# Performance work log

Measured on AMD Instinct MI355X. Metric: run time of the kernel, lower is better.

## Reference

```python
import jax, jax.numpy as jnp
import numpy as np

N = 50000      # num_nodes
E = 800000     # num_edges
D = 128        # node feature dim
ED = 64        # edge feature dim
H = 4          # num_heads
U = 32         # units per head (units*heads == 128)


def setup_inputs() -> dict:
    key = jax.random.key(0)
    ks = jax.random.split(key, 12)
    inputs = jax.random.normal(ks[0], (N, D), dtype=jnp.float32)
    # tf.math.segment_* requires sorted segment ids -> sort source row
    src = jnp.sort(jax.random.randint(ks[1], (E,), 0, N, dtype=jnp.int32))
    dst = jax.random.randint(ks[2], (E,), 0, N, dtype=jnp.int32)
    edge_index = jnp.stack([src, dst], axis=0)
    edge_features = jax.random.normal(ks[3], (E, ED), dtype=jnp.float32)
    def glorot(k, shape):
        lim = np.sqrt(6.0 / (shape[0] + shape[1]))
        return jax.random.uniform(k, shape, jnp.float32, -lim, lim)
    HU = H * U
    return {
        "inputs": inputs,
        "edge_index": edge_index,
        "edge_features": edge_features,
        "Wq": glorot(ks[4], (D, HU)), "bq": jnp.zeros((HU,), jnp.float32),
        "Wk": glorot(ks[5], (D, HU)), "bk": jnp.zeros((HU,), jnp.float32),
        "Wv": glorot(ks[6], (D, HU)), "bv": jnp.zeros((HU,), jnp.float32),
        "We": glorot(ks[7], (ED, HU)), "be": jnp.zeros((HU,), jnp.float32),
        "Wo": glorot(ks[8], (HU, U)), "bo": jnp.zeros((U,), jnp.float32),
    }


def _segment_softmax(scores, seg, num_segments):
    # numerically stable segmented softmax over ragged neighborhoods
    seg_max = jax.ops.segment_max(scores, seg, num_segments=num_segments)
    ex = jnp.exp(scores - seg_max[seg])
    seg_sum = jax.ops.segment_sum(ex, seg, num_segments=num_segments)
    return ex / seg_sum[seg]


def reference(inputs, edge_index, edge_features, Wq, bq, Wk, bk, Wv, bv, We, be, Wo, bo):
    n = inputs.shape[0]
    q = (inputs @ Wq + bq).reshape(n, H, U)
    k = (inputs @ Wk + bk).reshape(n, H, U)
    v = (inputs @ Wv + bv).reshape(n, H, U)
    src, dst = edge_index[0], edge_index[1]
    qi = q[src]                      # [E, H, U]
    kj = k[dst]                      # [E, H, U]
    scores = jnp.sum(qi * kj, axis=-1)   # [E, H]
    eh = (edge_features @ We + be).reshape(-1, H, U)
    scores = scores + jnp.sum(eh * kj, axis=-1)
    attn = _segment_softmax(scores, src, n)        # [E, H]
    attended = jax.ops.segment_sum(attn[..., None] * v[dst], src, num_segments=n)
    attended = attended.reshape(n, H * U)
    return jax.nn.relu(attended @ Wo + bo)
```

## Files before the change

kernel.cpp:

```cpp
#include <hip/hip_runtime.h>
#include <math.h>

#define N_NODES 50000
#define N_EDGES 800000
#define D_IN    128
#define ED_IN   64
#define HU      128
#define NH      4
#define UD      32

typedef float fx4 __attribute__((ext_vector_type(4)));
typedef short s16x8 __attribute__((ext_vector_type(8)));
typedef float f32x4 __attribute__((ext_vector_type(4)));

static __device__ __forceinline__ unsigned short f2bf(float f) {
  unsigned u = __float_as_uint(f);
  unsigned r = (u + 0x7FFFu + ((u >> 16) & 1u)) >> 16;
  return (unsigned short)r;
}
static __device__ __forceinline__ float bf_lo(unsigned u) {
  return __uint_as_float(u << 16);
}
static __device__ __forceinline__ float bf_hi(unsigned u) {
  return __uint_as_float(u & 0xFFFF0000u);
}
static __device__ __forceinline__ float bf2f(unsigned short h) {
  return __uint_as_float(((unsigned)h) << 16);
}
static __device__ __forceinline__ float dot8(float4 a0, float4 a1, uint4 kk) {
  return a0.x * bf_lo(kk.x) + a0.y * bf_hi(kk.x)
       + a0.z * bf_lo(kk.y) + a0.w * bf_hi(kk.y)
       + a1.x * bf_lo(kk.z) + a1.y * bf_hi(kk.z)
       + a1.z * bf_lo(kk.w) + a1.w * bf_hi(kk.w);
}
static __device__ __forceinline__ float4 f4add(float4 a, float4 b) {
  return make_float4(a.x + b.x, a.y + b.y, a.z + b.z, a.w + b.w);
}

__global__ __launch_bounds__(256) void offsets_kernel(
    const int* __restrict__ src, int* __restrict__ off) {
  const int e = blockIdx.x * 256 + threadIdx.x;
  if (e >= N_EDGES) return;
  const int s = src[e];
  const int prev = (e == 0) ? -1 : src[e - 1];
  for (int n = prev + 1; n <= s; ++n) off[n] = e;
  if (e == N_EDGES - 1)
    for (int n = s + 1; n <= N_NODES; ++n) off[n] = N_EDGES;
}

__global__ __launch_bounds__(256) void wepack_kernel(
    const float* __restrict__ We, unsigned short* __restrict__ wf) {
  const int fl = blockIdx.x * 256 + threadIdx.x;
  if (fl >= 16 * 64) return;
  const int f = fl >> 6, lane = fl & 63;
  const int nt = f >> 1, kh = f & 1;
  const int n = nt * 16 + (lane & 15);
  const int kbase = kh * 32 + (lane >> 4) * 8;
#pragma unroll
  for (int j = 0; j < 8; ++j)
    wf[fl * 8 + j] = f2bf(We[(kbase + j) * HU + n]);
}

__global__ __launch_bounds__(256) void wqkvpack_kernel(
    const float* __restrict__ Wq, const float* __restrict__ Wk,
    const float* __restrict__ Wv, unsigned short* __restrict__ wqkv) {
  const int fl = blockIdx.x * 256 + threadIdx.x;
  if (fl >= 96 * 64) return;
  const int f = fl >> 6, lane = fl & 63;
  const int proj = f >> 5, nt = (f >> 2) & 7, kf = f & 3;
  const float* W = proj == 0 ? Wq : (proj == 1 ? Wk : Wv);
  const int n = nt * 16 + (lane & 15);
  const int kb = kf * 32 + (lane >> 4) * 8;
#pragma unroll
  for (int j = 0; j < 8; ++j) {
    const float v = W[(kb + j) * HU + n];
    const unsigned short h = f2bf(v);
    wqkv[fl * 8 + j] = h;
    wqkv[96 * 64 * 8 + fl * 8 + j] = f2bf(v - bf2f(h));
  }
}

__global__ __launch_bounds__(256) void qkv_kernel(
    const float* __restrict__ x, const s16x8* __restrict__ wqkv,
    const float* __restrict__ bq, const float* __restrict__ be,
    const float* __restrict__ bk, const float* __restrict__ bv,
    float* __restrict__ q, unsigned short* __restrict__ kbf,
    unsigned short* __restrict__ vbf) {
  const int base = blockIdx.x * 16;
  const int t = threadIdx.x;
  const int w = t >> 6, l = t & 63;

  const float* xr = x + (long)(base + (l & 15)) * D_IN + (l >> 4) * 8;
  s16x8 Ah[4], Al[4];
#pragma unroll
  for (int kf = 0; kf < 4; ++kf) {
    const fx4 c0 = *(const fx4*)(xr + kf * 32);
    const fx4 c1 = *(const fx4*)(xr + kf * 32 + 4);
#pragma unroll
    for (int j = 0; j < 4; ++j) {
      const unsigned short h0 = f2bf(c0[j]);
      const unsigned short h1 = f2bf(c1[j]);
      Ah[kf][j] = (short)h0;     Al[kf][j] = (short)f2bf(c0[j] - bf2f(h0));
      Ah[kf][4 + j] = (short)h1; Al[kf][4 + j] = (short)f2bf(c1[j] - bf2f(h1));
    }
  }

#pragma unroll
  for (int i = 0; i < 6; ++i) {
    const int tt = w * 6 + i;
    const int proj = tt >> 3, nt = tt & 7;
    const int col = nt * 16 + (l & 15);
    f32x4 acc = (f32x4){0.f, 0.f, 0.f, 0.f};
#pragma unroll
    for (int kf = 0; kf < 4; ++kf) {
      const int fr = proj * 32 + nt * 4 + kf;
      const s16x8 Bh = wqkv[fr * 64 + l];
      const s16x8 Bl = wqkv[96 * 64 + fr * 64 + l];
      acc = __builtin_amdgcn_mfma_f32_16x16x32_bf16(Ah[kf], Bh, acc, 0, 0, 0);
      acc = __builtin_amdgcn_mfma_f32_16x16x32_bf16(Al[kf], Bh, acc, 0, 0, 0);
      acc = __builtin_amdgcn_mfma_f32_16x16x32_bf16(Ah[kf], Bl, acc, 0, 0, 0);
    }
    float bias;
    if (proj == 0)      bias = bq[col] + be[col];
    else if (proj == 1) bias = bk[col];
    else                bias = bv[col];
#pragma unroll
    for (int r = 0; r < 4; ++r) {
      const long node = base + (l >> 4) * 4 + r;
      const float val = acc[r] + bias;
      if (proj == 0)      q[node * HU + col] = val;
      else if (proj == 1) kbf[node * HU + col] = f2bf(val);
      else                vbf[node * HU + col] = f2bf(val);
    }
  }
}

__global__ __launch_bounds__(256) void score_kernel(
    const float* __restrict__ ef,
    const int* __restrict__ src, const int* __restrict__ dst,
    const float* __restrict__ q, const unsigned short* __restrict__ kbf,
    const s16x8* __restrict__ wf,
    float* __restrict__ scores) {
  __shared__ __align__(16) float ehs[4][16 * 64];
  const int t = threadIdx.x;
  const int w = t >> 6, l = t & 63;
  const long ebase = (long)blockIdx.x * 64;
  const int e = (int)(ebase + w * 16 + (l >> 2));
  const int hl = (l >> 1) & 1, half = l & 1;
  const int s = src[e], d = dst[e];

  const char* kbp = (const char*)kbf + (long)d * 256 + hl * 64 + half * 32;
  const uint4 k00 = *(const uint4*)(kbp);
  const uint4 k01 = *(const uint4*)(kbp + 16);
  const uint4 k10 = *(const uint4*)(kbp + 128);
  const uint4 k11 = *(const uint4*)(kbp + 144);

  const int arow = (int)(ebase + w * 16 + (l & 15));
  const fx4* ap = (const fx4*)(ef + (long)arow * ED_IN + (l >> 4) * 8);
  const fx4 a00 = __builtin_nontemporal_load(ap);
  const fx4 a01 = __builtin_nontemporal_load(ap + 1);
  const fx4 a10 = __builtin_nontemporal_load(ap + 8);
  const fx4 a11 = __builtin_nontemporal_load(ap + 9);
  s16x8 A0, A1;
  A0[0] = (short)f2bf(a00[0]); A0[1] = (short)f2bf(a00[1]);
  A0[2] = (short)f2bf(a00[2]); A0[3] = (short)f2bf(a00[3]);
  A0[4] = (short)f2bf(a01[0]); A0[5] = (short)f2bf(a01[1]);
  A0[6] = (short)f2bf(a01[2]); A0[7] = (short)f2bf(a01[3]);
  A1[0] = (short)f2bf(a10[0]); A1[1] = (short)f2bf(a10[1]);
  A1[2] = (short)f2bf(a10[2]); A1[3] = (short)f2bf(a10[3]);
  A1[4] = (short)f2bf(a11[0]); A1[5] = (short)f2bf(a11[1]);
  A1[6] = (short)f2bf(a11[2]); A1[7] = (short)f2bf(a11[3]);

  float* __restrict__ ehw = ehs[w];
  const int nb = l & 15, gbase = (l >> 4) * 4;
  const int rloc = l >> 2;
  const int swzr = (rloc & 7) << 4;

#pragma unroll
  for (int ph = 0; ph < 2; ++ph) {
    f32x4 acc[4];
#pragma unroll
    for (int ntl = 0; ntl < 4; ++ntl) acc[ntl] = (f32x4){0.f, 0.f, 0.f, 0.f};
#pragma unroll
    for (int ntl = 0; ntl < 4; ++ntl) {
      const int f = (ph * 4 + ntl) * 2;
      const s16x8 B0 = wf[(f + 0) * 64 + l];
      const s16x8 B1 = wf[(f + 1) * 64 + l];
      acc[ntl] = __builtin_amdgcn_mfma_f32_16x16x32_bf16(A0, B0, acc[ntl], 0, 0, 0);
      acc[ntl] = __builtin_amdgcn_mfma_f32_16x16x32_bf16(A1, B1, acc[ntl], 0, 0, 0);
    }

#pragma unroll
    for (int ntl = 0; ntl < 4; ++ntl) {
#pragma unroll
      for (int r = 0; r < 4; ++r) {
        const int m = gbase + r;
        const int b = (ntl * 16 + nb) * 4;
        ehw[(m * 256 + (b ^ ((m & 7) << 4))) >> 2] = acc[ntl][r];
      }
    }
    asm volatile("s_waitcnt lgkmcnt(0)" ::: "memory");
    __builtin_amdgcn_sched_barrier(0x30);

    const int h = ph * 2 + hl;
    const char* ehp = (const char*)(ehw + rloc * 64);
    const int cb = (l & 3) * 64;
    const float4 e0 = *(const float4*)(ehp + ((cb + 0)  ^ swzr));
    const float4 e1 = *(const float4*)(ehp + ((cb + 16) ^ swzr));
    const float4 e2 = *(const float4*)(ehp + ((cb + 32) ^ swzr));
    const float4 e3 = *(const float4*)(ehp + ((cb + 48) ^ swzr));

    const float4* qp = (const float4*)(q + (long)s * HU + h * 32 + half * 16);
    const float4 q0 = qp[0], q1 = qp[1], q2 = qp[2], q3 = qp[3];
    const uint4 k0 = ph ? k10 : k00;
    const uint4 k1 = ph ? k11 : k01;

    float p = dot8(f4add(q0, e0), f4add(q1, e1), k0)
            + dot8(f4add(q2, e2), f4add(q3, e3), k1);
    p += __shfl_xor(p, 1, 64);
    if (!half)
      __builtin_nontemporal_store(p, scores + (long)e * NH + h);

    asm volatile("s_waitcnt lgkmcnt(0)" ::: "memory");
    __builtin_amdgcn_sched_barrier(0x30);
  }
}

__global__ __launch_bounds__(256) void aggregate_kernel(
    const int* __restrict__ off, const int* __restrict__ dst,
    const float* __restrict__ scores, const unsigned* __restrict__ v2,
    const float* __restrict__ Wo, const float* __restrict__ bo,
    float* __restrict__ out) {
  const int wv = threadIdx.x >> 6, l = threadIdx.x & 63;
  const int n = blockIdx.x * 4 + wv;
  const int h = l >> 4, q16 = l & 15;
  __shared__ float att[4][HU];
  __shared__ __align__(16) float wos[HU * UD];

  {
    const fx4* wop = (const fx4*)Wo;
    fx4* wosp = (fx4*)wos;
#pragma unroll
    for (int r = 0; r < 4; ++r)
      wosp[threadIdx.x + 256 * r] = wop[threadIdx.x + 256 * r];
  }
  __syncthreads();

  const int start = off[n], end = off[n + 1];
  float m = -INFINITY, lsum = 0.f, a0 = 0.f, a1 = 0.f;
  for (int cs = start; cs < end; cs += 16) {
    const int e = cs + q16;
    const bool live = (e < end);
    const float sc = live ? __builtin_nontemporal_load(scores + (long)e * NH + h)
                          : -INFINITY;
    const int dl = live ? dst[e] : 0;
    float mc = sc;
#pragma unroll
    for (int o = 8; o > 0; o >>= 1) mc = fmaxf(mc, __shfl_xor(mc, o, 16));
    const float nm = fmaxf(m, mc);
    const float corr = __expf(m - nm);
    const float w = __expf(sc - nm);
    float ws = w;
#pragma unroll
    for (int o = 8; o > 0; o >>= 1) ws += __shfl_xor(ws, o, 16);
    lsum = lsum * corr + ws;
    a0 *= corr; a1 *= corr; m = nm;
#pragma unroll
    for (int j = 0; j < 16; ++j) {
      const float wj = __shfl(w, (l & 48) + j, 64);
      const int dj = __builtin_amdgcn_readlane(dl, j);
      const unsigned vr = v2[(long)dj * 64 + l];
      a0 += wj * bf_lo(vr);
      a1 += wj * bf_hi(vr);
    }
  }
  const float inv = (lsum > 0.f) ? 1.f / lsum : 0.f;
  att[wv][2 * l] = a0 * inv;
  att[wv][2 * l + 1] = a1 * inv;
  const int o = l & 31, half = l >> 5;
  float po = 0.f;
#pragma unroll
  for (int f = 0; f < 64; ++f)
    po += att[wv][half * 64 + f] * wos[(half * 64 + f) * UD + o];
  po += __shfl_down(po, 32, 64);
  if (l < 32) out[(long)n * UD + l] = fmaxf(po + bo[l], 0.f);
}

extern "C" void kernel_launch(void* const* d_in, const int* in_sizes, int n_in,
                              void* d_out, int out_size, void* d_ws, size_t ws_size,
                              hipStream_t stream) {
  const float* x  = (const float*)d_in[0];
  const int*   ei = (const int*)d_in[1];
  const float* ef = (const float*)d_in[2];
  const float* Wq = (const float*)d_in[3];
  const float* bq = (const float*)d_in[4];
  const float* Wk = (const float*)d_in[5];
  const float* bk = (const float*)d_in[6];
  const float* Wv = (const float*)d_in[7];
  const float* bv = (const float*)d_in[8];
  const float* We = (const float*)d_in[9];
  const float* be = (const float*)d_in[10];
  const float* Wo = (const float*)d_in[11];
  const float* bo = (const float*)d_in[12];
  float* out = (float*)d_out;

  const int* src = ei;
  const int* dst = ei + N_EDGES;

  float* q = (float*)d_ws;
  unsigned short* kbf = (unsigned short*)(q + (long)N_NODES * HU);
  unsigned short* vbf = kbf + (long)N_NODES * HU;
  float* scores = (float*)(vbf + (long)N_NODES * HU);
  int* off = (int*)(scores + (long)N_EDGES * NH);
  unsigned short* wf = (unsigned short*)(((uintptr_t)(off + N_NODES + 1) + 15)
                                         & ~(uintptr_t)15);
  unsigned short* wqkv = wf + 16 * 64 * 8;

  offsets_kernel<<<(N_EDGES + 255) / 256, 256, 0, stream>>>(src, off);
  wepack_kernel<<<4, 256, 0, stream>>>(We, wf);
  wqkvpack_kernel<<<24, 256, 0, stream>>>(Wq, Wk, Wv, wqkv);
  qkv_kernel<<<N_NODES / 16, 256, 0, stream>>>(x, (const s16x8*)wqkv,
                                               bq, be, bk, bv, q, kbf, vbf);
  score_kernel<<<N_EDGES / 64, 256, 0, stream>>>(ef, src, dst, q, kbf,
                                                 (const s16x8*)wf, scores);
  aggregate_kernel<<<N_NODES / 4, 256, 0, stream>>>(off, dst, scores,
                                                    (const unsigned*)vbf, Wo, bo, out);
}
```

Before: 461.4 us.

## Fuse edge score computation into per-node aggregation kernel

Merges the per-edge score kernel into the per-node segmented softmax/aggregation kernel, so each wave computes scores for its own node's 16-edge chunks with MFMA and passes them through shared memory. This removes the global scores buffer round trip and one kernel launch. Each chunk of a node with fewer than 16 edges still runs a full 16-edge MFMA tile, so work is wasted on partial chunks. Wo is also read directly from global memory instead of being staged into shared memory.

```diff
diff --git a/kernel.cpp b/kernel.cpp
--- a/kernel.cpp
+++ b/kernel.cpp
@@ -135,125 +135,108 @@
   }
 }
 
-__global__ __launch_bounds__(256) void score_kernel(
-    const float* __restrict__ ef,
-    const int* __restrict__ src, const int* __restrict__ dst,
-    const float* __restrict__ q, const unsigned short* __restrict__ kbf,
-    const s16x8* __restrict__ wf,
-    float* __restrict__ scores) {
-  __shared__ __align__(16) float ehs[4][16 * 64];
-  const int t = threadIdx.x;
-  const int w = t >> 6, l = t & 63;
-  const long ebase = (long)blockIdx.x * 64;
-  const int e = (int)(ebase + w * 16 + (l >> 2));
-  const int hl = (l >> 1) & 1, half = l & 1;
-  const int s = src[e], d = dst[e];
-
-  const char* kbp = (const char*)kbf + (long)d * 256 + hl * 64 + half * 32;
-  const uint4 k00 = *(const uint4*)(kbp);
-  const uint4 k01 = *(const uint4*)(kbp + 16);
-  const uint4 k10 = *(const uint4*)(kbp + 128);
-  const uint4 k11 = *(const uint4*)(kbp + 144);
-
-  const int arow = (int)(ebase + w * 16 + (l & 15));
-  const fx4* ap = (const fx4*)(ef + (long)arow * ED_IN + (l >> 4) * 8);
-  const fx4 a00 = __builtin_nontemporal_load(ap);
-  const fx4 a01 = __builtin_nontemporal_load(ap + 1);
-  const fx4 a10 = __builtin_nontemporal_load(ap + 8);
-  const fx4 a11 = __builtin_nontemporal_load(ap + 9);
-  s16x8 A0, A1;
-  A0[0] = (short)f2bf(a00[0]); A0[1] = (short)f2bf(a00[1]);
-  A0[2] = (short)f2bf(a00[2]); A0[3] = (short)f2bf(a00[3]);
-  A0[4] = (short)f2bf(a01[0]); A0[5] = (short)f2bf(a01[1]);
-  A0[6] = (short)f2bf(a01[2]); A0[7] = (short)f2bf(a01[3]);
-  A1[0] = (short)f2bf(a10[0]); A1[1] = (short)f2bf(a10[1]);
-  A1[2] = (short)f2bf(a10[2]); A1[3] = (short)f2bf(a10[3]);
-  A1[4] = (short)f2bf(a11[0]); A1[5] = (short)f2bf(a11[1]);
-  A1[6] = (short)f2bf(a11[2]); A1[7] = (short)f2bf(a11[3]);
-
-  float* __restrict__ ehw = ehs[w];
-  const int nb = l & 15, gbase = (l >> 4) * 4;
-  const int rloc = l >> 2;
-  const int swzr = (rloc & 7) << 4;
-
-#pragma unroll
-  for (int ph = 0; ph < 2; ++ph) {
-    f32x4 acc[4];
-#pragma unroll
-    for (int ntl = 0; ntl < 4; ++ntl) acc[ntl] = (f32x4){0.f, 0.f, 0.f, 0.f};
-#pragma unroll
-    for (int ntl = 0; ntl < 4; ++ntl) {
-      const int f = (ph * 4 + ntl) * 2;
-      const s16x8 B0 = wf[(f + 0) * 64 + l];
-      const s16x8 B1 = wf[(f + 1) * 64 + l];
-      acc[ntl] = __builtin_amdgcn_mfma_f32_16x16x32_bf16(A0, B0, acc[ntl], 0, 0, 0);
-      acc[ntl] = __builtin_amdgcn_mfma_f32_16x16x32_bf16(A1, B1, acc[ntl], 0, 0, 0);
-    }
-
-#pragma unroll
-    for (int ntl = 0; ntl < 4; ++ntl) {
-#pragma unroll
-      for (int r = 0; r < 4; ++r) {
-        const int m = gbase + r;
-        const int b = (ntl * 16 + nb) * 4;
-        ehw[(m * 256 + (b ^ ((m & 7) << 4))) >> 2] = acc[ntl][r];
-      }
-    }
-    asm volatile("s_waitcnt lgkmcnt(0)" ::: "memory");
-    __builtin_amdgcn_sched_barrier(0x30);
-
-    const int h = ph * 2 + hl;
-    const char* ehp = (const char*)(ehw + rloc * 64);
-    const int cb = (l & 3) * 64;
-    const float4 e0 = *(const float4*)(ehp + ((cb + 0)  ^ swzr));
-    const float4 e1 = *(const float4*)(ehp + ((cb + 16) ^ swzr));
-    const float4 e2 = *(const float4*)(ehp + ((cb + 32) ^ swzr));
-    const float4 e3 = *(const float4*)(ehp + ((cb + 48) ^ swzr));
-
-    const float4* qp = (const float4*)(q + (long)s * HU + h * 32 + half * 16);
-    const float4 q0 = qp[0], q1 = qp[1], q2 = qp[2], q3 = qp[3];
-    const uint4 k0 = ph ? k10 : k00;
-    const uint4 k1 = ph ? k11 : k01;
-
-    float p = dot8(f4add(q0, e0), f4add(q1, e1), k0)
-            + dot8(f4add(q2, e2), f4add(q3, e3), k1);
-    p += __shfl_xor(p, 1, 64);
-    if (!half)
-      __builtin_nontemporal_store(p, scores + (long)e * NH + h);
-
-    asm volatile("s_waitcnt lgkmcnt(0)" ::: "memory");
-    __builtin_amdgcn_sched_barrier(0x30);
-  }
-}
-
-__global__ __launch_bounds__(256) void aggregate_kernel(
+__global__ __launch_bounds__(256) void fused_kernel(
     const int* __restrict__ off, const int* __restrict__ dst,
-    const float* __restrict__ scores, const unsigned* __restrict__ v2,
+    const float* __restrict__ ef, const float* __restrict__ q,
+    const unsigned short* __restrict__ kbf, const s16x8* __restrict__ wf,
+    const unsigned* __restrict__ v2,
     const float* __restrict__ Wo, const float* __restrict__ bo,
     float* __restrict__ out) {
-  const int wv = threadIdx.x >> 6, l = threadIdx.x & 63;
+  __shared__ __align__(16) float ehs[4][16 * 64];
+  __shared__ float scr[4][NH][16];
+  __shared__ float att[4][HU];
+  const int t = threadIdx.x;
+  const int wv = t >> 6, l = t & 63;
   const int n = blockIdx.x * 4 + wv;
   const int h = l >> 4, q16 = l & 15;
-  __shared__ float att[4][HU];
-  __shared__ __align__(16) float wos[HU * UD];
-
-  {
-    const fx4* wop = (const fx4*)Wo;
-    fx4* wosp = (fx4*)wos;
-#pragma unroll
-    for (int r = 0; r < 4; ++r)
-      wosp[threadIdx.x + 256 * r] = wop[threadIdx.x + 256 * r];
-  }
-  __syncthreads();
+  const int rloc = l >> 2, hl = (l >> 1) & 1, half = l & 1;
+  const int swzr = (rloc & 7) << 4;
+  const int nb = l & 15, gbase = (l >> 4) * 4;
+  float* __restrict__ ehw = ehs[wv];
 
   const int start = off[n], end = off[n + 1];
   float m = -INFINITY, lsum = 0.f, a0 = 0.f, a1 = 0.f;
+
   for (int cs = start; cs < end; cs += 16) {
+    const int ar0 = cs + (l & 15);
+    const int ar = ar0 < N_EDGES ? ar0 : N_EDGES - 1;
+    const fx4* ap = (const fx4*)(ef + (long)ar * ED_IN + (l >> 4) * 8);
+    const fx4 a00 = __builtin_nontemporal_load(ap);
+    const fx4 a01 = __builtin_nontemporal_load(ap + 1);
+    const fx4 a10 = __builtin_nontemporal_load(ap + 8);
+    const fx4 a11 = __builtin_nontemporal_load(ap + 9);
+
+    const int ed0 = cs + rloc;
+    const int edot = ed0 < N_EDGES ? ed0 : N_EDGES - 1;
+    const int ddot = dst[edot];
+    const char* kbp = (const char*)kbf + (long)ddot * 256 + hl * 64 + half * 32;
+    const uint4 k00 = *(const uint4*)(kbp);
+    const uint4 k01 = *(const uint4*)(kbp + 16);
+    const uint4 k10 = *(const uint4*)(kbp + 128);
+    const uint4 k11 = *(const uint4*)(kbp + 144);
+
     const int e = cs + q16;
-    const bool live = (e < end);
-    const float sc = live ? __builtin_nontemporal_load(scores + (long)e * NH + h)
-                          : -INFINITY;
+    const bool live = e < end;
     const int dl = live ? dst[e] : 0;
+
+    s16x8 A0, A1;
+    A0[0] = (short)f2bf(a00[0]); A0[1] = (short)f2bf(a00[1]);
+    A0[2] = (short)f2bf(a00[2]); A0[3] = (short)f2bf(a00[3]);
+    A0[4] = (short)f2bf(a01[0]); A0[5] = (short)f2bf(a01[1]);
+    A0[6] = (short)f2bf(a01[2]); A0[7] = (short)f2bf(a01[3]);
+    A1[0] = (short)f2bf(a10[0]); A1[1] = (short)f2bf(a10[1]);
+    A1[2] = (short)f2bf(a10[2]); A1[3] = (short)f2bf(a10[3]);
+    A1[4] = (short)f2bf(a11[0]); A1[5] = (short)f2bf(a11[1]);
+    A1[6] = (short)f2bf(a11[2]); A1[7] = (short)f2bf(a11[3]);
+
+#pragma unroll
+    for (int ph = 0; ph < 2; ++ph) {
+      f32x4 acc[4];
+#pragma unroll
+      for (int ntl = 0; ntl < 4; ++ntl) acc[ntl] = (f32x4){0.f, 0.f, 0.f, 0.f};
+#pragma unroll
+      for (int ntl = 0; ntl < 4; ++ntl) {
+        const int f = (ph * 4 + ntl) * 2;
+        const s16x8 B0 = wf[(f + 0) * 64 + l];
+        const s16x8 B1 = wf[(f + 1) * 64 + l];
+        acc[ntl] = __builtin_amdgcn_mfma_f32_16x16x32_bf16(A0, B0, acc[ntl], 0, 0, 0);
+        acc[ntl] = __builtin_amdgcn_mfma_f32_16x16x32_bf16(A1, B1, acc[ntl], 0, 0, 0);
+      }
+#pragma unroll
+      for (int ntl = 0; ntl < 4; ++ntl) {
+#pragma unroll
+        for (int r = 0; r < 4; ++r) {
+          const int mm = gbase + r;
+          const int b = (ntl * 16 + nb) * 4;
+          ehw[(mm * 256 + (b ^ ((mm & 7) << 4))) >> 2] = acc[ntl][r];
+        }
+      }
+      asm volatile("s_waitcnt lgkmcnt(0)" ::: "memory");
+      __builtin_amdgcn_sched_barrier(0x30);
+
+      const int hh = ph * 2 + hl;
+      const char* ehp = (const char*)(ehw + rloc * 64);
+      const int cb = (l & 3) * 64;
+      const float4 e0 = *(const float4*)(ehp + ((cb + 0)  ^ swzr));
+      const float4 e1 = *(const float4*)(ehp + ((cb + 16) ^ swzr));
+      const float4 e2 = *(const float4*)(ehp + ((cb + 32) ^ swzr));
+      const float4 e3 = *(const float4*)(ehp + ((cb + 48) ^ swzr));
+
+      const float4* qp = (const float4*)(q + (long)n * HU + hh * 32 + half * 16);
+      const float4 q0 = qp[0], q1 = qp[1], q2 = qp[2], q3 = qp[3];
+      const uint4 kk0 = ph ? k10 : k00;
+      const uint4 kk1 = ph ? k11 : k01;
+
+      float p = dot8(f4add(q0, e0), f4add(q1, e1), kk0)
+              + dot8(f4add(q2, e2), f4add(q3, e3), kk1);
+      p += __shfl_xor(p, 1, 64);
+      if (!half) scr[wv][hh][rloc] = p;
+
+      asm volatile("s_waitcnt lgkmcnt(0)" ::: "memory");
+      __builtin_amdgcn_sched_barrier(0x30);
+    }
+
+    const float sc = live ? scr[wv][h][q16] : -INFINITY;
     float mc = sc;
 #pragma unroll
     for (int o = 8; o > 0; o >>= 1) mc = fmaxf(mc, __shfl_xor(mc, o, 16));
@@ -274,14 +257,15 @@
       a1 += wj * bf_hi(vr);
     }
   }
+
   const float inv = (lsum > 0.f) ? 1.f / lsum : 0.f;
   att[wv][2 * l] = a0 * inv;
   att[wv][2 * l + 1] = a1 * inv;
-  const int o = l & 31, half = l >> 5;
+  const int o = l & 31, oh = l >> 5;
   float po = 0.f;
 #pragma unroll
   for (int f = 0; f < 64; ++f)
-    po += att[wv][half * 64 + f] * wos[(half * 64 + f) * UD + o];
+    po += att[wv][oh * 64 + f] * Wo[(oh * 64 + f) * UD + o];
   po += __shfl_down(po, 32, 64);
   if (l < 32) out[(long)n * UD + l] = fmaxf(po + bo[l], 0.f);
 }
@@ -310,8 +294,7 @@
   float* q = (float*)d_ws;
   unsigned short* kbf = (unsigned short*)(q + (long)N_NODES * HU);
   unsigned short* vbf = kbf + (long)N_NODES * HU;
-  float* scores = (float*)(vbf + (long)N_NODES * HU);
-  int* off = (int*)(scores + (long)N_EDGES * NH);
+  int* off = (int*)(vbf + (long)N_NODES * HU);
   unsigned short* wf = (unsigned short*)(((uintptr_t)(off + N_NODES + 1) + 15)
                                          & ~(uintptr_t)15);
   unsigned short* wqkv = wf + 16 * 64 * 8;
@@ -321,8 +304,7 @@
   wqkvpack_kernel<<<24, 256, 0, stream>>>(Wq, Wk, Wv, wqkv);
   qkv_kernel<<<N_NODES / 16, 256, 0, stream>>>(x, (const s16x8*)wqkv,
                                                bq, be, bk, bv, q, kbf, vbf);
-  score_kernel<<<N_EDGES / 64, 256, 0, stream>>>(ef, src, dst, q, kbf,
-                                                 (const s16x8*)wf, scores);
-  aggregate_kernel<<<N_NODES / 4, 256, 0, stream>>>(off, dst, scores,
-                                                    (const unsigned*)vbf, Wo, bo, out);
-}
+  fused_kernel<<<N_NODES / 4, 256, 0, stream>>>(off, dst, ef, q, kbf,
+                                                (const s16x8*)wf,
+                                                (const unsigned*)vbf, Wo, bo, out);
+}
```

Result: slower. 550.2 us (+19.3%).
